# Kernel optimization log

Measured on AMD Instinct MI355X. Metric: run time of the kernel, lower is better.

Reference implementation:

```python
import jax, jax.numpy as jnp
import numpy as np

N_DIALOGS = 60
DIA_LEN = 100
N = N_DIALOGS * DIA_LEN  # 6000 utterances total
D_IN = 512
D_OUT = 512


def setup_inputs() -> dict:
    key = jax.random.key(0)
    k1, k2, k3, k4 = jax.random.split(key, 4)
    inputs = jax.random.normal(k1, (N, D_IN), dtype=jnp.float32)
    # per-dialog lengths (concrete host array; defines static graph structure)
    dia_len = np.full((N_DIALOGS,), DIA_LEN, dtype=np.int64)
    # one-hot speaker mask [N, 1, 2]; qmask[j,0,0]==1 -> speaker0 else speaker1
    sp = jax.random.randint(k2, (N,), 0, 2)
    qmask = jnp.zeros((N, 1, 2), jnp.int64).at[jnp.arange(N), 0, sp].set(1)
    W = jax.random.normal(k3, (D_OUT, D_IN), dtype=jnp.float32) / np.sqrt(D_IN)
    b = jax.random.normal(k4, (D_OUT,), dtype=jnp.float32) * 0.01
    return {"inputs": inputs, "dia_len": dia_len, "qmask": qmask, "W": W, "b": b}


def build_adj(inputs, dia_len, qmask):
    # Vectorized equivalent of message_passing_directed_speaker:
    # adj = I; edge (i,j) iff i,j in same dialog, same speaker, and consecutive
    # among that speaker's utterances; weight = 1 - arccos(clip(cos,-1,1))/pi.
    n = inputs.shape[0]
    dia_len_np = np.asarray(dia_len)
    did = jnp.asarray(np.repeat(np.arange(len(dia_len_np)), dia_len_np))  # dialog id per node
    sp0 = qmask[:, 0, 0] == 1  # True -> speaker0
    cs0 = jnp.cumsum(sp0.astype(jnp.int32))
    cs1 = jnp.cumsum((~sp0).astype(jnp.int32))
    csel = jnp.where(sp0, cs0, cs1)  # running count of own speaker
    idx = jnp.arange(n)
    # j>i, same dialog, same speaker, no same-speaker utterance strictly between
    upper = ((did[None, :] == did[:, None])
             & (sp0[None, :] == sp0[:, None])
             & (csel[None, :] - csel[:, None] == 1)
             & (idx[None, :] > idx[:, None]))
    edge = upper | upper.T
    # pairwise cosine similarity (cossim returns 0 when a norm is 0)
    nrm = jnp.sqrt(jnp.sum(inputs * inputs, axis=-1))  # [N]
    denom = nrm[:, None] * nrm[None, :]
    dots = inputs @ inputs.T  # [N, N]
    cos = jnp.where(denom > 0, dots / jnp.where(denom > 0, denom, 1.0), 0.0)
    cos_safe = jnp.where(edge, jnp.clip(cos, -1.0, 1.0), 0.0)
    w = 1.0 - jnp.arccos(cos_safe) / jnp.pi
    return jnp.where(edge, w, 0.0) + jnp.eye(n, dtype=inputs.dtype)


def reference(inputs, dia_len, qmask, W, b):
    adj = build_adj(inputs, dia_len, qmask)  # [N, N]
    x = adj @ inputs                          # [N, D_IN]
    return x @ W.T + b                        # [N, D_OUT]
```

## Files before the change

### kernel.cpp

```cpp
#include <hip/hip_runtime.h>
#include <hip/hip_bf16.h>

#define N_NODES 6000
#define N_DIA   60
#define DIA     100
#define DDIM    512
#define LDA     520

typedef short short8   __attribute__((ext_vector_type(8)));
typedef float floatx4  __attribute__((ext_vector_type(4)));

__device__ __forceinline__ unsigned short f2bf(float f) {
    unsigned int u = __float_as_uint(f);
    unsigned int r = (u + 0x7fffu + ((u >> 16) & 1u)) >> 16;
    return (unsigned short)r;
}

__device__ __forceinline__ float wave_reduce_sum(float v) {
    #pragma unroll
    for (int off = 32; off > 0; off >>= 1) v += __shfl_xor(v, off, 64);
    return v;
}

__global__ __launch_bounds__(256) void edge_kernel(
    const float* __restrict__ x, const int* __restrict__ qmask,
    const float* __restrict__ W, int* __restrict__ nxt, int* __restrict__ prv,
    float* __restrict__ wn, unsigned short* __restrict__ wbf)
{
    int bid = blockIdx.x;
    int tid = threadIdx.x;
    if (bid >= N_NODES / 4) {
        int base = (bid - N_NODES / 4) * 2048 + tid * 8;
        float4 a = *(const float4*)(W + base);
        float4 b = *(const float4*)(W + base + 4);
        union { unsigned short u[8]; short8 v; } o;
        o.u[0]=f2bf(a.x); o.u[1]=f2bf(a.y); o.u[2]=f2bf(a.z); o.u[3]=f2bf(a.w);
        o.u[4]=f2bf(b.x); o.u[5]=f2bf(b.y); o.u[6]=f2bf(b.z); o.u[7]=f2bf(b.w);
        *(short8*)(wbf + base) = o.v;
        return;
    }
    int wv = tid >> 6, lane = tid & 63;
    int i = bid * 4 + wv;
    int sp = qmask[2 * i];
    int dstart = (i / DIA) * DIA;
    int dend   = dstart + DIA;

    int cand = i + 1 + lane;
    unsigned long long b1 = __ballot(cand < dend && qmask[2 * cand] == sp);
    int j = -1;
    if (b1) j = i + __ffsll(b1);
    else {
        int c2 = i + 65 + lane;
        unsigned long long b2 = __ballot(lane < 35 && c2 < dend && qmask[2 * c2] == sp);
        if (b2) j = i + 64 + __ffsll(b2);
    }
    int candp = i - 1 - lane;
    unsigned long long p1 = __ballot(candp >= dstart && qmask[2 * candp] == sp);
    int p = -1;
    if (p1) p = i - __ffsll(p1);
    else {
        int pc2 = i - 65 - lane;
        unsigned long long p2 = __ballot(lane < 35 && pc2 >= dstart && qmask[2 * pc2] == sp);
        if (p2) p = i - 64 - __ffsll(p2);
    }

    float w = 0.0f;
    if (j >= 0) {
        const float* ri = x + (size_t)i * DDIM + lane * 8;
        const float* rj = x + (size_t)j * DDIM + lane * 8;
        float4 a0 = *(const float4*)(ri);
        float4 a1 = *(const float4*)(ri + 4);
        float4 b0 = *(const float4*)(rj);
        float4 b1 = *(const float4*)(rj + 4);
        float d  = a0.x*b0.x + a0.y*b0.y + a0.z*b0.z + a0.w*b0.w
                 + a1.x*b1.x + a1.y*b1.y + a1.z*b1.z + a1.w*b1.w;
        float ni = a0.x*a0.x + a0.y*a0.y + a0.z*a0.z + a0.w*a0.w
                 + a1.x*a1.x + a1.y*a1.y + a1.z*a1.z + a1.w*a1.w;
        float nj = b0.x*b0.x + b0.y*b0.y + b0.z*b0.z + b0.w*b0.w
                 + b1.x*b1.x + b1.y*b1.y + b1.z*b1.z + b1.w*b1.w;
        d  = wave_reduce_sum(d);
        ni = wave_reduce_sum(ni);
        nj = wave_reduce_sum(nj);
        float dn = ni * nj;
        float c = (dn > 0.0f) ? (d * __frsqrt_rn(dn)) : 0.0f;
        c = fminf(1.0f, fmaxf(-1.0f, c));
        w = 1.0f - acosf(c) * 0.3183098861837907f;
    }
    if (lane == 0) { nxt[i] = j; prv[i] = p; wn[i] = w; }
}

__global__ __launch_bounds__(512) void build_gemm(
    const float* __restrict__ x, const int* __restrict__ nxt,
    const int* __restrict__ prv, const float* __restrict__ wn,
    const unsigned short* __restrict__ wbf, const float* __restrict__ bias,
    float* __restrict__ out)
{
    __shared__ unsigned short As[64 * LDA];
    int tid = threadIdx.x;
    int wv = tid >> 6, lane = tid & 63;
    int m0 = blockIdx.x * 64;

    #pragma unroll 2
    for (int t = 0; t < 8; ++t) {
        int rr = wv * 8 + t;
        int i = m0 + rr;
        unsigned short* dst = As + rr * LDA + lane * 8;
        if (i >= N_NODES) {
            *(short8*)dst = (short8)0;
            continue;
        }
        int j = nxt[i];
        int p = prv[i];
        float wi = (j >= 0) ? wn[i] : 0.0f;
        float wp = (p >= 0) ? wn[p] : 0.0f;
        const float* ri = x + (size_t)i * DDIM + lane * 8;
        float acc[8];
        {
            float4 a = *(const float4*)(ri);
            float4 b = *(const float4*)(ri + 4);
            acc[0]=a.x; acc[1]=a.y; acc[2]=a.z; acc[3]=a.w;
            acc[4]=b.x; acc[5]=b.y; acc[6]=b.z; acc[7]=b.w;
        }
        if (j >= 0) {
            const float* rj = x + (size_t)j * DDIM + lane * 8;
            float4 a = *(const float4*)(rj);
            float4 b = *(const float4*)(rj + 4);
            acc[0]+=wi*a.x; acc[1]+=wi*a.y; acc[2]+=wi*a.z; acc[3]+=wi*a.w;
            acc[4]+=wi*b.x; acc[5]+=wi*b.y; acc[6]+=wi*b.z; acc[7]+=wi*b.w;
        }
        if (p >= 0) {
            const float* rp = x + (size_t)p * DDIM + lane * 8;
            float4 a = *(const float4*)(rp);
            float4 b = *(const float4*)(rp + 4);
            acc[0]+=wp*a.x; acc[1]+=wp*a.y; acc[2]+=wp*a.z; acc[3]+=wp*a.w;
            acc[4]+=wp*b.x; acc[5]+=wp*b.y; acc[6]+=wp*b.z; acc[7]+=wp*b.w;
        }
        union { unsigned short u[8]; short8 v; } o;
        #pragma unroll
        for (int q = 0; q < 8; ++q) o.u[q] = f2bf(acc[q]);
        *(short8*)dst = o.v;
    }
    __syncthreads();

    int n0 = blockIdx.y * 256 + wv * 32;
    int fr = lane & 15;
    int kq = (lane >> 4) * 8;
    floatx4 acc[4][2] = {};
    const unsigned short* As_base = As + fr * LDA + kq;
    const unsigned short* bb = wbf + (size_t)(n0 + fr) * DDIM + kq;

    #pragma unroll 2
    for (int k = 0; k < DDIM; k += 32) {
        short8 af[4], bfv[2];
        #pragma unroll
        for (int ms = 0; ms < 4; ++ms)
            af[ms] = *(const short8*)(As_base + ms * 16 * LDA + k);
        #pragma unroll
        for (int ns = 0; ns < 2; ++ns)
            bfv[ns] = *(const short8*)(bb + (size_t)ns * 16 * DDIM + k);
        #pragma unroll
        for (int ms = 0; ms < 4; ++ms)
            #pragma unroll
            for (int ns = 0; ns < 2; ++ns)
                acc[ms][ns] = __builtin_amdgcn_mfma_f32_16x16x32_bf16(
                    af[ms], bfv[ns], acc[ms][ns], 0, 0, 0);
    }

    int col = lane & 15;
    int rbase = (lane >> 4) * 4;
    #pragma unroll
    for (int ms = 0; ms < 4; ++ms) {
        #pragma unroll
        for (int ns = 0; ns < 2; ++ns) {
            int n = n0 + ns * 16 + col;
            float bv = bias[n];
            #pragma unroll
            for (int r = 0; r < 4; ++r) {
                int m = m0 + ms * 16 + rbase + r;
                if (m < N_NODES)
                    out[(size_t)m * DDIM + n] = acc[ms][ns][r] + bv;
            }
        }
    }
}

extern "C" void kernel_launch(void* const* d_in, const int* in_sizes, int n_in,
                              void* d_out, int out_size, void* d_ws, size_t ws_size,
                              hipStream_t stream) {
    const float* inputs = (const float*)d_in[0];
    const int* qmask   = (const int*)d_in[2];
    const float* W     = (const float*)d_in[3];
    const float* bias  = (const float*)d_in[4];
    float* out = (float*)d_out;

    char* ws = (char*)d_ws;
    unsigned short* wbf = (unsigned short*)ws;
    float* wn  = (float*)(ws + 524288);
    int*   nxt = (int*)(ws + 524288 + 24576);
    int*   prv = (int*)(ws + 524288 + 2 * 24576);

    edge_kernel<<<dim3(N_NODES / 4 + 128), 256, 0, stream>>>(
        inputs, qmask, W, nxt, prv, wn, wbf);
    build_gemm <<<dim3(94, 2),            512, 0, stream>>>(
        inputs, nxt, prv, wn, wbf, bias, out);
}
```

Measured before the change: 94.89 us.

## Fuse edge discovery and cosine weights into the build-GEMM kernel

Edge finding (next/previous same-speaker neighbour via per-dialog ballot bitmasks) and the arccos cosine weights are now computed inside the GEMM kernel's A-tile construction. This removes the separate edge kernel and its workspace round trip. The W bf16 cast moves to its own small kernel. The M tile drops from 64 to 32 rows, doubling the grid to 376 blocks for better CU fill. The cost is computing each edge weight twice (once from each endpoint), extra wave reductions per row, and half as much W reuse per block.

```diff
diff --git a/kernel.cpp b/kernel.cpp
--- a/kernel.cpp
+++ b/kernel.cpp
@@ -22,118 +22,128 @@
     return v;
 }
 
-__global__ __launch_bounds__(256) void edge_kernel(
+__global__ __launch_bounds__(256) void wcast_kernel(
+    const float* __restrict__ W, unsigned short* __restrict__ wbf)
+{
+    int base = blockIdx.x * 2048 + threadIdx.x * 8;
+    float4 a = *(const float4*)(W + base);
+    float4 b = *(const float4*)(W + base + 4);
+    union { unsigned short u[8]; short8 v; } o;
+    o.u[0]=f2bf(a.x); o.u[1]=f2bf(a.y); o.u[2]=f2bf(a.z); o.u[3]=f2bf(a.w);
+    o.u[4]=f2bf(b.x); o.u[5]=f2bf(b.y); o.u[6]=f2bf(b.z); o.u[7]=f2bf(b.w);
+    *(short8*)(wbf + base) = o.v;
+}
+
+__global__ __launch_bounds__(512, 4) void fused_kernel(
     const float* __restrict__ x, const int* __restrict__ qmask,
-    const float* __restrict__ W, int* __restrict__ nxt, int* __restrict__ prv,
-    float* __restrict__ wn, unsigned short* __restrict__ wbf)
-{
-    int bid = blockIdx.x;
-    int tid = threadIdx.x;
-    if (bid >= N_NODES / 4) {
-        int base = (bid - N_NODES / 4) * 2048 + tid * 8;
-        float4 a = *(const float4*)(W + base);
-        float4 b = *(const float4*)(W + base + 4);
-        union { unsigned short u[8]; short8 v; } o;
-        o.u[0]=f2bf(a.x); o.u[1]=f2bf(a.y); o.u[2]=f2bf(a.z); o.u[3]=f2bf(a.w);
-        o.u[4]=f2bf(b.x); o.u[5]=f2bf(b.y); o.u[6]=f2bf(b.z); o.u[7]=f2bf(b.w);
-        *(short8*)(wbf + base) = o.v;
-        return;
-    }
-    int wv = tid >> 6, lane = tid & 63;
-    int i = bid * 4 + wv;
-    int sp = qmask[2 * i];
-    int dstart = (i / DIA) * DIA;
-    int dend   = dstart + DIA;
-
-    int cand = i + 1 + lane;
-    unsigned long long b1 = __ballot(cand < dend && qmask[2 * cand] == sp);
-    int j = -1;
-    if (b1) j = i + __ffsll(b1);
-    else {
-        int c2 = i + 65 + lane;
-        unsigned long long b2 = __ballot(lane < 35 && c2 < dend && qmask[2 * c2] == sp);
-        if (b2) j = i + 64 + __ffsll(b2);
-    }
-    int candp = i - 1 - lane;
-    unsigned long long p1 = __ballot(candp >= dstart && qmask[2 * candp] == sp);
-    int p = -1;
-    if (p1) p = i - __ffsll(p1);
-    else {
-        int pc2 = i - 65 - lane;
-        unsigned long long p2 = __ballot(lane < 35 && pc2 >= dstart && qmask[2 * pc2] == sp);
-        if (p2) p = i - 64 - __ffsll(p2);
-    }
-
-    float w = 0.0f;
-    if (j >= 0) {
-        const float* ri = x + (size_t)i * DDIM + lane * 8;
-        const float* rj = x + (size_t)j * DDIM + lane * 8;
-        float4 a0 = *(const float4*)(ri);
-        float4 a1 = *(const float4*)(ri + 4);
-        float4 b0 = *(const float4*)(rj);
-        float4 b1 = *(const float4*)(rj + 4);
-        float d  = a0.x*b0.x + a0.y*b0.y + a0.z*b0.z + a0.w*b0.w
-                 + a1.x*b1.x + a1.y*b1.y + a1.z*b1.z + a1.w*b1.w;
-        float ni = a0.x*a0.x + a0.y*a0.y + a0.z*a0.z + a0.w*a0.w
-                 + a1.x*a1.x + a1.y*a1.y + a1.z*a1.z + a1.w*a1.w;
-        float nj = b0.x*b0.x + b0.y*b0.y + b0.z*b0.z + b0.w*b0.w
-                 + b1.x*b1.x + b1.y*b1.y + b1.z*b1.z + b1.w*b1.w;
-        d  = wave_reduce_sum(d);
-        ni = wave_reduce_sum(ni);
-        nj = wave_reduce_sum(nj);
-        float dn = ni * nj;
-        float c = (dn > 0.0f) ? (d * __frsqrt_rn(dn)) : 0.0f;
-        c = fminf(1.0f, fmaxf(-1.0f, c));
-        w = 1.0f - acosf(c) * 0.3183098861837907f;
-    }
-    if (lane == 0) { nxt[i] = j; prv[i] = p; wn[i] = w; }
-}
-
-__global__ __launch_bounds__(512) void build_gemm(
-    const float* __restrict__ x, const int* __restrict__ nxt,
-    const int* __restrict__ prv, const float* __restrict__ wn,
     const unsigned short* __restrict__ wbf, const float* __restrict__ bias,
     float* __restrict__ out)
 {
-    __shared__ unsigned short As[64 * LDA];
+    __shared__ unsigned short As[32 * LDA];
     int tid = threadIdx.x;
     int wv = tid >> 6, lane = tid & 63;
-    int m0 = blockIdx.x * 64;
-
-    #pragma unroll 2
-    for (int t = 0; t < 8; ++t) {
-        int rr = wv * 8 + t;
+    int m0 = blockIdx.x * 32;
+
+    int cached_d = -1;
+    unsigned long long sm_a = 0, sm_b = 0;
+    #pragma unroll
+    for (int t = 0; t < 4; ++t) {
+        int rr = wv * 4 + t;
         int i = m0 + rr;
         unsigned short* dst = As + rr * LDA + lane * 8;
         if (i >= N_NODES) {
             *(short8*)dst = (short8)0;
             continue;
         }
-        int j = nxt[i];
-        int p = prv[i];
-        float wi = (j >= 0) ? wn[i] : 0.0f;
-        float wp = (p >= 0) ? wn[p] : 0.0f;
+        int d = i / DIA;
+        int dstart = d * DIA;
+        if (d != cached_d) {
+            sm_a = __ballot(qmask[2 * (dstart + lane)] == 1);
+            sm_b = __ballot(lane < 36 && qmask[2 * (dstart + 64 + lane)] == 1);
+            cached_d = d;
+        }
+        int pos = i - dstart;
+        int sp = (pos < 64) ? (int)((sm_a >> pos) & 1)
+                            : (int)((sm_b >> (pos - 64)) & 1);
+        unsigned long long Ma = sp ? sm_a : ~sm_a;
+        unsigned long long Mb = sp ? sm_b : (~sm_b & 0xFFFFFFFFFULL);
+
+        int j = -1;
+        {
+            unsigned long long aa = (pos < 64) ? (Ma & ~((2ULL << pos) - 1)) : 0ULL;
+            if (aa) j = dstart + __builtin_ctzll(aa);
+            else {
+                unsigned long long bb = (pos >= 64)
+                    ? (Mb & ~((2ULL << (pos - 64)) - 1)) : Mb;
+                if (bb) j = dstart + 64 + __builtin_ctzll(bb);
+            }
+        }
+        int p = -1;
+        {
+            unsigned long long bb = (pos > 64)
+                ? (Mb & ((1ULL << (pos - 64)) - 1)) : 0ULL;
+            if (bb) p = dstart + 64 + (63 - __builtin_clzll(bb));
+            else {
+                unsigned long long aa = (pos >= 64) ? Ma
+                    : (pos ? (Ma & ((1ULL << pos) - 1)) : 0ULL);
+                if (aa) p = dstart + (63 - __builtin_clzll(aa));
+            }
+        }
+
         const float* ri = x + (size_t)i * DDIM + lane * 8;
-        float acc[8];
-        {
-            float4 a = *(const float4*)(ri);
-            float4 b = *(const float4*)(ri + 4);
-            acc[0]=a.x; acc[1]=a.y; acc[2]=a.z; acc[3]=a.w;
-            acc[4]=b.x; acc[5]=b.y; acc[6]=b.z; acc[7]=b.w;
-        }
+        float4 ia = *(const float4*)(ri);
+        float4 ib = *(const float4*)(ri + 4);
+        float ni = ia.x*ia.x + ia.y*ia.y + ia.z*ia.z + ia.w*ia.w
+                 + ib.x*ib.x + ib.y*ib.y + ib.z*ib.z + ib.w*ib.w;
+        float4 ja, jb; float dij = 0.0f, nj = 0.0f;
         if (j >= 0) {
             const float* rj = x + (size_t)j * DDIM + lane * 8;
-            float4 a = *(const float4*)(rj);
-            float4 b = *(const float4*)(rj + 4);
-            acc[0]+=wi*a.x; acc[1]+=wi*a.y; acc[2]+=wi*a.z; acc[3]+=wi*a.w;
-            acc[4]+=wi*b.x; acc[5]+=wi*b.y; acc[6]+=wi*b.z; acc[7]+=wi*b.w;
-        }
+            ja = *(const float4*)(rj);
+            jb = *(const float4*)(rj + 4);
+            dij = ia.x*ja.x + ia.y*ja.y + ia.z*ja.z + ia.w*ja.w
+                + ib.x*jb.x + ib.y*jb.y + ib.z*jb.z + ib.w*jb.w;
+            nj  = ja.x*ja.x + ja.y*ja.y + ja.z*ja.z + ja.w*ja.w
+                + jb.x*jb.x + jb.y*jb.y + jb.z*jb.z + jb.w*jb.w;
+        }
+        float4 pa, pb; float dpi = 0.0f, np_ = 0.0f;
         if (p >= 0) {
             const float* rp = x + (size_t)p * DDIM + lane * 8;
-            float4 a = *(const float4*)(rp);
-            float4 b = *(const float4*)(rp + 4);
-            acc[0]+=wp*a.x; acc[1]+=wp*a.y; acc[2]+=wp*a.z; acc[3]+=wp*a.w;
-            acc[4]+=wp*b.x; acc[5]+=wp*b.y; acc[6]+=wp*b.z; acc[7]+=wp*b.w;
+            pa = *(const float4*)(rp);
+            pb = *(const float4*)(rp + 4);
+            dpi = ia.x*pa.x + ia.y*pa.y + ia.z*pa.z + ia.w*pa.w
+                + ib.x*pb.x + ib.y*pb.y + ib.z*pb.z + ib.w*pb.w;
+            np_ = pa.x*pa.x + pa.y*pa.y + pa.z*pa.z + pa.w*pa.w
+                + pb.x*pb.x + pb.y*pb.y + pb.z*pb.z + pb.w*pb.w;
+        }
+        ni = wave_reduce_sum(ni);
+        float wj = 0.0f, wp = 0.0f;
+        if (j >= 0) {
+            dij = wave_reduce_sum(dij);
+            nj  = wave_reduce_sum(nj);
+            float dn = ni * nj;
+            float c = (dn > 0.0f) ? (dij * __frsqrt_rn(dn)) : 0.0f;
+            c = fminf(1.0f, fmaxf(-1.0f, c));
+            wj = 1.0f - acosf(c) * 0.3183098861837907f;
+        }
+        if (p >= 0) {
+            dpi = wave_reduce_sum(dpi);
+            np_ = wave_reduce_sum(np_);
+            float dn = ni * np_;
+            float c = (dn > 0.0f) ? (dpi * __frsqrt_rn(dn)) : 0.0f;
+            c = fminf(1.0f, fmaxf(-1.0f, c));
+            wp = 1.0f - acosf(c) * 0.3183098861837907f;
+        }
+
+        float acc[8];
+        acc[0]=ia.x; acc[1]=ia.y; acc[2]=ia.z; acc[3]=ia.w;
+        acc[4]=ib.x; acc[5]=ib.y; acc[6]=ib.z; acc[7]=ib.w;
+        if (j >= 0) {
+            acc[0]+=wj*ja.x; acc[1]+=wj*ja.y; acc[2]+=wj*ja.z; acc[3]+=wj*ja.w;
+            acc[4]+=wj*jb.x; acc[5]+=wj*jb.y; acc[6]+=wj*jb.z; acc[7]+=wj*jb.w;
+        }
+        if (p >= 0) {
+            acc[0]+=wp*pa.x; acc[1]+=wp*pa.y; acc[2]+=wp*pa.z; acc[3]+=wp*pa.w;
+            acc[4]+=wp*pb.x; acc[5]+=wp*pb.y; acc[6]+=wp*pb.z; acc[7]+=wp*pb.w;
         }
         union { unsigned short u[8]; short8 v; } o;
         #pragma unroll
@@ -145,40 +155,38 @@
     int n0 = blockIdx.y * 256 + wv * 32;
     int fr = lane & 15;
     int kq = (lane >> 4) * 8;
-    floatx4 acc[4][2] = {};
+    floatx4 acc2[2][2] = {};
     const unsigned short* As_base = As + fr * LDA + kq;
     const unsigned short* bb = wbf + (size_t)(n0 + fr) * DDIM + kq;
 
-    #pragma unroll 2
+    #pragma unroll 4
     for (int k = 0; k < DDIM; k += 32) {
-        short8 af[4], bfv[2];
+        short8 af[2], bfv[2];
+        af[0] = *(const short8*)(As_base + k);
+        af[1] = *(const short8*)(As_base + 16 * LDA + k);
+        bfv[0] = *(const short8*)(bb + k);
+        bfv[1] = *(const short8*)(bb + (size_t)16 * DDIM + k);
         #pragma unroll
-        for (int ms = 0; ms < 4; ++ms)
-            af[ms] = *(const short8*)(As_base + ms * 16 * LDA + k);
-        #pragma unroll
-        for (int ns = 0; ns < 2; ++ns)
-            bfv[ns] = *(const short8*)(bb + (size_t)ns * 16 * DDIM + k);
-        #pragma unroll
-        for (int ms = 0; ms < 4; ++ms)
+        for (int ms = 0; ms < 2; ++ms)
             #pragma unroll
             for (int ns = 0; ns < 2; ++ns)
-                acc[ms][ns] = __builtin_amdgcn_mfma_f32_16x16x32_bf16(
-                    af[ms], bfv[ns], acc[ms][ns], 0, 0, 0);
+                acc2[ms][ns] = __builtin_amdgcn_mfma_f32_16x16x32_bf16(
+                    af[ms], bfv[ns], acc2[ms][ns], 0, 0, 0);
     }
 
     int col = lane & 15;
     int rbase = (lane >> 4) * 4;
     #pragma unroll
-    for (int ms = 0; ms < 4; ++ms) {
+    for (int ns = 0; ns < 2; ++ns) {
+        int n = n0 + ns * 16 + col;
+        float bv = bias[n];
         #pragma unroll
-        for (int ns = 0; ns < 2; ++ns) {
-            int n = n0 + ns * 16 + col;
-            float bv = bias[n];
+        for (int ms = 0; ms < 2; ++ms) {
             #pragma unroll
             for (int r = 0; r < 4; ++r) {
                 int m = m0 + ms * 16 + rbase + r;
                 if (m < N_NODES)
-                    out[(size_t)m * DDIM + n] = acc[ms][ns][r] + bv;
+                    out[(size_t)m * DDIM + n] = acc2[ms][ns][r] + bv;
             }
         }
     }
@@ -193,14 +201,8 @@
     const float* bias  = (const float*)d_in[4];
     float* out = (float*)d_out;
 
-    char* ws = (char*)d_ws;
-    unsigned short* wbf = (unsigned short*)ws;
-    float* wn  = (float*)(ws + 524288);
-    int*   nxt = (int*)(ws + 524288 + 24576);
-    int*   prv = (int*)(ws + 524288 + 2 * 24576);
-
-    edge_kernel<<<dim3(N_NODES / 4 + 128), 256, 0, stream>>>(
-        inputs, qmask, W, nxt, prv, wn, wbf);
-    build_gemm <<<dim3(94, 2),            512, 0, stream>>>(
-        inputs, nxt, prv, wn, wbf, bias, out);
-}
+    unsigned short* wbf = (unsigned short*)d_ws;
+
+    wcast_kernel<<<128, 256, 0, stream>>>(W, wbf);
+    fused_kernel<<<dim3(188, 2), 512, 0, stream>>>(inputs, qmask, wbf, bias, out);
+}
```

Result: slower. 98.42 us (+3.7%).
